# Kernel tuning notes

Measured on AMD Instinct MI355X. Metric: run time of the kernel, lower is better.

## Reference

```python
import math
import jax, jax.numpy as jnp
import numpy as np

B, N, DIM, H = 2, 4096, 1024, 16
DH = DIM // H
LEVELS = int(math.log2(N))
SCALE = 1.0 / math.sqrt(DH)


def build_lookup_table(seq_len):
    """Replicates build_hierarchical_index_lookup_table (numpy, static)."""
    levels = int(math.log2(seq_len))
    total_nodes = 2 * seq_len - 1
    max_valid = total_nodes - 2
    idx = np.full((seq_len, levels), -1, dtype=np.int32)
    cm = np.zeros((seq_len, levels), dtype=bool)
    for n in range(seq_len):
        nc = n
        for l in range(levels):
            if l == 0:
                pair = nc
                nn = nc ^ 1
            else:
                pair = nc // 2 + seq_len
                nn = pair ^ 1  # (nc//2 + seq_len) ^ 1 per Python precedence
            if nn > max_valid:
                break
            if pair < nn:
                cm[n, l] = True  # neighbor is to the right -> causally masked
            idx[n, l] = nn
            nc = nn
    return idx, cm


def setup_inputs() -> dict:
    key = jax.random.key(0)
    ks = jax.random.split(key, 12)
    w = lambda k: (jax.random.normal(k, (DIM, DIM), dtype=jnp.float32) * 0.02)
    idx_np, cm_np = build_lookup_table(N)
    return {
        "x": jax.random.normal(ks[0], (B, N, DIM), dtype=jnp.float32),
        "Wq_y": w(ks[1]), "Wk_y": w(ks[2]), "Wv_y": w(ks[3]),
        "Wo_y": w(ks[4]), "bo_y": jnp.zeros((DIM,), jnp.float32),
        "Wq_x": w(ks[5]), "Wk_x": w(ks[6]), "Wv_x": w(ks[7]),
        "Wo_x": w(ks[8]), "bo_x": jnp.zeros((DIM,), jnp.float32),
        "idx_map": jnp.asarray(idx_np, dtype=jnp.int32),       # [N, LEVELS]
        "causal_mask": jnp.asarray(cm_np, dtype=jnp.bool_),    # [N, LEVELS]
    }


def _heads(t):
    b, n, _ = t.shape
    return t.reshape(b, n, H, DH)


def _forward(x, Wq_y, Wk_y, Wv_y, Wo_y, bo_y, Wq_x, Wk_x, Wv_x, Wo_x, bo_x,
             idx_map, causal_mask):
    # ---- stage 1: build parent nodes level by level (online 2-child softmax merge)
    nodes = [x]  # leaves: [B, N, DIM]; parents appended level by level
    cur = x
    for _ in range(LEVELS):
        pre = 0.5 * (cur[:, 0::2] + cur[:, 1::2])     # parent query source [B,P,DIM]
        q = _heads(pre @ Wq_y)                        # [B,P,H,DH]
        k = _heads(cur @ Wk_y)                        # [B,C,H,DH]
        v = _heads(cur @ Wv_y)
        s0 = jnp.einsum('bphd,bphd->bph', q, k[:, 0::2]) * SCALE
        s1 = jnp.einsum('bphd,bphd->bph', q, k[:, 1::2]) * SCALE
        m = jnp.maximum(s0, s1)
        e0 = jnp.exp(s0 - m)
        e1 = jnp.exp(s1 - m)
        denom = e0 + e1 + 1e-9
        parent = ((e0 / denom)[..., None] * v[:, 0::2]
                  + (e1 / denom)[..., None] * v[:, 1::2])   # [B,P,H,DH]
        bp, pp = parent.shape[0], parent.shape[1]
        parent = parent.reshape(bp, pp, DIM) @ Wo_y + bo_y
        nodes.append(parent)
        cur = parent
    h_all = jnp.concatenate(nodes, axis=1)            # [B, 2N-1, DIM]

    # ---- stage 2: fused multi-level gather attention over self + neighbors
    Q = _heads(x @ Wq_x)                              # leaf queries [B,N,H,DH]
    K_all = _heads(h_all @ Wk_x)                      # [B,2N-1,H,DH]
    V_all = _heads(h_all @ Wv_x)

    k_cross = jnp.take(K_all, idx_map, axis=1)        # [B,N,LEVELS,H,DH]
    v_cross = jnp.take(V_all, idx_map, axis=1)

    s_self = jnp.einsum('bnhd,bnhd->bnh', Q, K_all[:, :N]) * SCALE   # [B,N,H]
    s_cross = jnp.einsum('bnhd,bnlhd->bnhl', Q, k_cross) * SCALE     # [B,N,H,L]
    neg_inf = jnp.float32(-jnp.inf)
    s_cross = jnp.where(causal_mask[None, :, None, :], neg_inf, s_cross)

    scores = jnp.concatenate([s_self[..., None], s_cross], axis=-1)  # [B,N,H,L+1]
    w = jax.nn.softmax(scores, axis=-1)
    out = (w[..., 0:1] * V_all[:, :N]
           + jnp.einsum('bnhl,bnlhd->bnhd', w[..., 1:], v_cross))    # [B,N,H,DH]
    return out.reshape(B, N, DIM) @ Wo_x + bo_x


def reference(x, Wq_y, Wk_y, Wv_y, Wo_y, bo_y, Wq_x, Wk_x, Wv_x, Wo_x, bo_x,
              idx_map, causal_mask):
    return _forward(x, Wq_y, Wk_y, Wv_y, Wo_y, bo_y,
                    Wq_x, Wk_x, Wv_x, Wo_x, bo_x, idx_map, causal_mask)
```

## Files before the change

### kernel.cpp

```cpp
#include <hip/hip_runtime.h>
#include <stdint.h>

#define H_NODES 8191
#define NN 4096
#define DIMC 1024

typedef __bf16 bf16x8 __attribute__((ext_vector_type(8)));
typedef float f32x4 __attribute__((ext_vector_type(4)));

__device__ __forceinline__ float b2f(ushort u) {
  union { uint32_t i; float f; } x; x.i = ((uint32_t)u) << 16; return x.f;
}
__device__ __forceinline__ ushort f2b(float f) {
  union { float f; uint32_t i; } x; x.f = f;
  uint32_t r = x.i + 0x7FFFu + ((x.i >> 16) & 1u);
  return (ushort)(r >> 16);
}
__device__ __forceinline__ void load16f(const ushort* p, float* f) {
  const uint32_t* w = (const uint32_t*)p;
  #pragma unroll
  for (int i = 0; i < 8; ++i) {
    uint32_t v = w[i];
    f[2 * i]     = b2f((ushort)(v & 0xffff));
    f[2 * i + 1] = b2f((ushort)(v >> 16));
  }
}
__device__ __forceinline__ void store16b(ushort* p, const float* f) {
  uint32_t w[8];
  #pragma unroll
  for (int i = 0; i < 8; ++i)
    w[i] = (uint32_t)f2b(f[2 * i]) | ((uint32_t)f2b(f[2 * i + 1]) << 16);
  *(uint4*)p = *(const uint4*)&w[0];
  *(uint4*)(p + 8) = *(const uint4*)&w[4];
}

struct WPtrs { const float* w[8]; };

__global__ void __launch_bounds__(256) transpose_w_k(WPtrs wp, ushort* __restrict__ dst) {
  __shared__ float t[32][33];
  const float* src = wp.w[blockIdx.z];
  int c0 = blockIdx.x * 32, r0 = blockIdx.y * 32;
  int tx = threadIdx.x, ty = threadIdx.y;
  #pragma unroll
  for (int i = ty; i < 32; i += 8)
    t[i][tx] = src[(long)(r0 + i) * DIMC + c0 + tx];
  __syncthreads();
  ushort* d = dst + (long)blockIdx.z * DIMC * DIMC;
  #pragma unroll
  for (int i = ty; i < 32; i += 8)
    d[(long)(c0 + i) * DIMC + r0 + tx] = f2b(t[tx][i]);
}

__global__ void __launch_bounds__(256) cvt_x_k(const float* __restrict__ x, ushort* __restrict__ h) {
  long t = (long)blockIdx.x * 256 + threadIdx.x;
  long i = t << 2;
  if (i >= (long)2 * NN * DIMC) return;
  long row = i >> 10;
  int col = (int)(i & 1023);
  long b = row >> 12;
  long n = row & 4095;
  float4 v = *(const float4*)(x + i);
  ushort* d = h + ((b * H_NODES + n) << 10) + col;
  uint2 pk;
  pk.x = (uint32_t)f2b(v.x) | ((uint32_t)f2b(v.y) << 16);
  pk.y = (uint32_t)f2b(v.z) | ((uint32_t)f2b(v.w) << 16);
  *(uint2*)d = pk;
}

__global__ void __launch_bounds__(256) avg_pairs_k(const ushort* __restrict__ h,
    ushort* __restrict__ pre, int P, int offL) {
  long t = (long)blockIdx.x * 256 + threadIdx.x;
  if (t >= (long)2 * P * 128) return;
  int dblk = (int)(t & 127);
  long r = t >> 7;
  int b = (r >= P) ? 1 : 0;
  int p = (int)(r - (long)b * P);
  const ushort* c = h + (((long)(b * H_NODES + offL + 2 * p)) << 10) + dblk * 8;
  const uint4 a0 = *(const uint4*)c;
  const uint4 a1 = *(const uint4*)(c + DIMC);
  const uint32_t* pa = (const uint32_t*)&a0;
  const uint32_t* pb = (const uint32_t*)&a1;
  uint32_t outw[4];
  #pragma unroll
  for (int i = 0; i < 4; ++i) {
    float x0 = b2f((ushort)(pa[i] & 0xffff)), x1 = b2f((ushort)(pa[i] >> 16));
    float y0 = b2f((ushort)(pb[i] & 0xffff)), y1 = b2f((ushort)(pb[i] >> 16));
    ushort r0 = f2b(0.5f * (x0 + y0)), r1 = f2b(0.5f * (x1 + y1));
    outw[i] = (uint32_t)r0 | ((uint32_t)r1 << 16);
  }
  *(uint4*)(pre + (((long)(b * P + p)) << 10) + dblk * 8) = *(const uint4*)outw;
}

struct GemmDesc {
  const ushort* A; long sAb;
  const ushort* Bt;
  const float* bias;
  void* C; long sCb; int ldc;
  int M; int outMode;
  int tX, tY;
  ushort* preC;
  long sPreB;
};

__device__ __forceinline__ void stage_tile(const GemmDesc& d, const ushort* Ab,
    int row0, int col0, ushort* lA, ushort* lB, int kt, int wave, int lane) {
  #pragma unroll
  for (int j = 0; j < 2; ++j) {
    int s = wave * 128 + j * 64 + lane;
    int r = s >> 2;
    int g = (s & 3) ^ ((r >> 1) & 3);
    int gr = row0 + r; gr = (gr < d.M) ? gr : (d.M - 1);
    const ushort* srcA = Ab + (long)gr * DIMC + kt * 32 + g * 8;
    __builtin_amdgcn_global_load_lds(
        (const __attribute__((address_space(1))) void*)(uintptr_t)srcA,
        (__attribute__((address_space(3))) void*)(uint32_t)(uintptr_t)(lA + (wave * 128 + j * 64) * 8),
        16, 0, 0);
    const ushort* srcB = d.Bt + (long)(col0 + r) * DIMC + kt * 32 + g * 8;
    __builtin_amdgcn_global_load_lds(
        (const __attribute__((address_space(1))) void*)(uintptr_t)srcB,
        (__attribute__((address_space(3))) void*)(uint32_t)(uintptr_t)(lB + (wave * 128 + j * 64) * 8),
        16, 0, 0);
  }
}

__device__ __forceinline__ void gemm_tile(const GemmDesc& d, int bz, int row0, int col0,
    ushort* lA, ushort* lB, int tid) {
  const ushort* Ab = d.A + (long)bz * d.sAb;
  int wave = tid >> 6, lane = tid & 63;
  int wr = wave >> 1, wc = wave & 1;

  f32x4 acc[4][4];
  #pragma unroll
  for (int m = 0; m < 4; ++m)
    #pragma unroll
    for (int n = 0; n < 4; ++n) acc[m][n] = (f32x4){0.f, 0.f, 0.f, 0.f};

  int rr = lane & 15, g4 = lane >> 4;
  for (int kt = 0; kt < 32; ++kt) {
    stage_tile(d, Ab, row0, col0, lA, lB, kt, wave, lane);
    __syncthreads();
    bf16x8 af[4], bfr[4];
    #pragma unroll
    for (int m = 0; m < 4; ++m) {
      int r = wr * 64 + m * 16 + rr;
      int slot = g4 ^ ((r >> 1) & 3);
      af[m] = *reinterpret_cast<const bf16x8*>(&lA[r * 32 + slot * 8]);
    }
    #pragma unroll
    for (int n = 0; n < 4; ++n) {
      int r = wc * 64 + n * 16 + rr;
      int slot = g4 ^ ((r >> 1) & 3);
      bfr[n] = *reinterpret_cast<const bf16x8*>(&lB[r * 32 + slot * 8]);
    }
    #pragma unroll
    for (int m = 0; m < 4; ++m)
      #pragma unroll
      for (int n = 0; n < 4; ++n)
        acc[m][n] = __builtin_amdgcn_mfma_f32_16x16x32_bf16(af[m], bfr[n], acc[m][n], 0, 0, 0);
    __syncthreads();
  }

  int rq = lane >> 4;
  #pragma unroll
  for (int n = 0; n < 4; ++n) {
    int col = col0 + wc * 64 + n * 16 + rr;
    float bv = d.bias ? d.bias[col] : 0.0f;
    #pragma unroll
    for (int m = 0; m < 4; ++m) {
      int gr0 = row0 + wr * 64 + m * 16 + rq * 4;
      float vv[4];
      #pragma unroll
      for (int r = 0; r < 4; ++r) vv[r] = acc[m][n][r] + bv;
      #pragma unroll
      for (int r = 0; r < 4; ++r) {
        int gr = gr0 + r;
        if (gr < d.M) {
          long o = (long)bz * d.sCb + (long)gr * d.ldc + col;
          if (d.outMode == 2) ((float*)d.C)[o] = vv[r];
          else ((ushort*)d.C)[o] = f2b(vv[r]);
        }
      }
      if (d.preC) {
        #pragma unroll
        for (int r = 0; r < 4; r += 2) {
          int gr = gr0 + r;
          if (gr + 1 < d.M)
            d.preC[(long)bz * d.sPreB + (long)(gr >> 1) * DIMC + col] =
                f2b(0.5f * (vv[r] + vv[r + 1]));
        }
      }
    }
  }
}

__global__ void __launch_bounds__(256, 4) gemm_multi(GemmDesc d0, GemmDesc d1, int t0) {
  __shared__ __align__(16) ushort lA[4096];
  __shared__ __align__(16) ushort lB[4096];
  int t = blockIdx.x;
  const GemmDesc& d = (t < t0) ? d0 : d1;
  int u = (t < t0) ? t : t - t0;
  int per = d.tX * d.tY;
  int bz = u / per;
  int rem = u - bz * per;
  int ty = rem / d.tX;
  int tx = rem - ty * d.tX;
  gemm_tile(d, bz, tx * 128, ty * 128, lA, lB, threadIdx.x);
}

__global__ void __launch_bounds__(256) merge_y2_k(const ushort* __restrict__ q,
    const ushort* __restrict__ kv, ushort* __restrict__ outp, int P) {
  int wave = threadIdx.x >> 6, lane = threadIdx.x & 63;
  long w = (long)blockIdx.x * 4 + wave;
  if (w >= (long)2 * P) return;
  int b = (w >= P) ? 1 : 0;
  int p = (int)(w - (long)b * P);
  const ushort* qp = q + (((long)(b * P + p)) << 10) + lane * 16;
  const ushort* kvb = kv + ((long)(b * 2 * P + 2 * p)) * 2048;
  float qf[16], k0f[16], k1f[16];
  load16f(qp, qf);
  load16f(kvb + lane * 16, k0f);
  load16f(kvb + 2048 + lane * 16, k1f);
  float d0 = 0.f, d1 = 0.f;
  #pragma unroll
  for (int j = 0; j < 16; ++j) { d0 += qf[j] * k0f[j]; d1 += qf[j] * k1f[j]; }
  d0 += __shfl_xor(d0, 1); d0 += __shfl_xor(d0, 2);
  d1 += __shfl_xor(d1, 1); d1 += __shfl_xor(d1, 2);
  float s0 = d0 * 0.125f, s1 = d1 * 0.125f;
  float mm = fmaxf(s0, s1);
  float e0 = expf(s0 - mm), e1 = expf(s1 - mm);
  float inv = 1.0f / (e0 + e1 + 1e-9f);
  float w0 = e0 * inv, w1 = e1 * inv;
  float v0f[16], v1f[16], ov[16];
  load16f(kvb + 1024 + lane * 16, v0f);
  load16f(kvb + 2048 + 1024 + lane * 16, v1f);
  #pragma unroll
  for (int j = 0; j < 16; ++j) ov[j] = w0 * v0f[j] + w1 * v1f[j];
  store16b(outp + (((long)(b * P + p)) << 10) + lane * 16, ov);
}

__global__ void __launch_bounds__(256) attn_x2_k(const ushort* __restrict__ Q,
    const ushort* __restrict__ KV, ushort* __restrict__ outp) {
  int wave = threadIdx.x >> 6, lane = threadIdx.x & 63;
  long w = (long)blockIdx.x * 4 + wave;
  int n = (int)(w & 4095);
  int b = (int)(w >> 12);
  const ushort* KVb = KV + (long)b * H_NODES * 2048;
  float qf[16];
  load16f(Q + (((long)b * NN + n) << 10) + lane * 16, qf);
  int nb[13];
  nb[0] = n;
  #pragma unroll
  for (int l = 0; l < 12; ++l) nb[1 + l] = (8192 - (8192 >> l)) + ((n >> l) ^ 1);
  float s[13];
  #pragma unroll
  for (int i = 0; i < 13; ++i) {
    float kf[16];
    load16f(KVb + (long)nb[i] * 2048 + lane * 16, kf);
    float d = 0.f;
    #pragma unroll
    for (int j = 0; j < 16; ++j) d += qf[j] * kf[j];
    d += __shfl_xor(d, 1);
    d += __shfl_xor(d, 2);
    s[i] = d * 0.125f;
  }
  #pragma unroll
  for (int l = 0; l < 12; ++l)
    if (((n >> l) & 1) == 0) s[1 + l] = -__builtin_inff();
  float mm = s[0];
  #pragma unroll
  for (int i = 1; i < 13; ++i) mm = fmaxf(mm, s[i]);
  float e[13], sum = 0.f;
  #pragma unroll
  for (int i = 0; i < 13; ++i) { e[i] = expf(s[i] - mm); sum += e[i]; }
  float inv = 1.0f / sum;
  float ov[16];
  #pragma unroll
  for (int j = 0; j < 16; ++j) ov[j] = 0.f;
  #pragma unroll
  for (int i = 0; i < 13; ++i) {
    float wgt = e[i] * inv;
    float vf[16];
    load16f(KVb + (long)nb[i] * 2048 + 1024 + lane * 16, vf);
    #pragma unroll
    for (int j = 0; j < 16; ++j) ov[j] += wgt * vf[j];
  }
  store16b(outp + (((long)b * NN + n) << 10) + lane * 16, ov);
}

extern "C" void kernel_launch(void* const* d_in, const int* in_sizes, int n_in,
                              void* d_out, int out_size, void* d_ws, size_t ws_size,
                              hipStream_t stream) {
  const float* x    = (const float*)d_in[0];
  const float* Wq_y = (const float*)d_in[1];
  const float* Wk_y = (const float*)d_in[2];
  const float* Wv_y = (const float*)d_in[3];
  const float* Wo_y = (const float*)d_in[4];
  const float* bo_y = (const float*)d_in[5];
  const float* Wq_x = (const float*)d_in[6];
  const float* Wk_x = (const float*)d_in[7];
  const float* Wv_x = (const float*)d_in[8];
  const float* Wo_x = (const float*)d_in[9];
  const float* bo_x = (const float*)d_in[10];

  ushort* wt  = (ushort*)d_ws;
  ushort* h   = wt + (size_t)8 * 1024 * 1024;
  ushort* reg = h + (size_t)2 * H_NODES * DIMC;
  ushort* Qx   = reg;
  ushort* KVa  = Qx + (size_t)2 * 4096 * DIMC;
  ushort* aout = KVa + (size_t)2 * H_NODES * 2048;
  ushort* preB = aout;
  ushort* qbB  = preB + (size_t)2 * 2048 * DIMC;
  ushort* kv1B = qbB + (size_t)2 * 2048 * DIMC;
  ushort* mrgB = kv1B + (size_t)2 * 4096 * 2048;
  ushort* preS = preB;
  ushort* qbS  = qbB;
  ushort* kv1S = kv1B;
  ushort* mrgS = mrgB;

  size_t wsElems = (size_t)8 * 1024 * 1024 + (size_t)2 * H_NODES * DIMC +
                   (size_t)2 * 4096 * DIMC + (size_t)2 * H_NODES * 2048 +
                   ((size_t)2 * 2048 * DIMC * 2 + (size_t)2 * 4096 * 2048 +
                    (size_t)2 * 2048 * DIMC);
  if (ws_size < wsElems * 2) return;

  WPtrs wp;
  wp.w[0] = Wq_y; wp.w[1] = Wk_y; wp.w[2] = Wv_y; wp.w[3] = Wo_y;
  wp.w[4] = Wq_x; wp.w[5] = Wk_x; wp.w[6] = Wv_x; wp.w[7] = Wo_x;
  transpose_w_k<<<dim3(32, 32, 8), dim3(32, 8), 0, stream>>>(wp, wt);
  cvt_x_k<<<8192, 256, 0, stream>>>(x, h);
  avg_pairs_k<<<(2 * 2048 * 128 + 255) / 256, 256, 0, stream>>>(h, preB, 2048, 0);

  auto mk128 = [](const ushort* A, long sAb, const ushort* Bt, const float* bias,
                  void* C, long sCb, int ldc, int M, int outMode, int tY) {
    GemmDesc d; d.A = A; d.sAb = sAb; d.Bt = Bt; d.bias = bias; d.C = C; d.sCb = sCb;
    d.ldc = ldc; d.M = M; d.outMode = outMode; d.tX = (M + 127) / 128; d.tY = tY;
    d.preC = nullptr; d.sPreB = 0;
    return d;
  };
  auto kvSub = [&](long start, int len) {
    return mk128(h + start * DIMC, (long)H_NODES * DIMC, wt + (size_t)5 * 1024 * 1024,
                 nullptr, KVa + start * 2048, (long)H_NODES * 2048, 2048, len, 0, 16);
  };
  auto qSub = [&](long start, int len) {
    return mk128(h + start * DIMC, (long)H_NODES * DIMC, wt + (size_t)4 * 1024 * 1024,
                 nullptr, Qx + start * DIMC, (long)4096 * DIMC, DIMC, len, 0, 8);
  };

  for (int l = 0; l < 12; ++l) {
    int P = NN >> (l + 1);
    int offL = 8192 - (8192 >> l);
    int offP = 8192 - (8192 >> (l + 1));
    ushort* pre = (l >= 3) ? preS : preB;
    ushort* qb  = (l >= 3) ? qbS  : qbB;
    ushort* kv1 = (l >= 3) ? kv1S : kv1B;
    ushort* mrg = (l >= 3) ? mrgS : mrgB;

    GemmDesc dq  = mk128(pre, (long)P * DIMC, wt, nullptr,
                         qb, (long)P * DIMC, DIMC, P, 0, 8);
    GemmDesc dkv = mk128(h + (long)offL * DIMC, (long)H_NODES * DIMC,
                         wt + (size_t)1 * 1024 * 1024, nullptr,
                         kv1, (long)2 * P * 2048, 2048, 2 * P, 0, 16);
    int t0 = dq.tX * dq.tY * 2;
    gemm_multi<<<t0 + dkv.tX * dkv.tY * 2, 256, 0, stream>>>(dq, dkv, t0);

    merge_y2_k<<<(2 * P + 3) / 4, 256, 0, stream>>>(qb, kv1, mrg, P);

    GemmDesc dgo = mk128(mrg, (long)P * DIMC, wt + (size_t)3 * 1024 * 1024, bo_y,
                         h + (long)offP * DIMC, (long)H_NODES * DIMC, DIMC, P, 1, 8);
    if (l < 11) {
      dgo.preC = (l >= 2) ? preS : preB;
      dgo.sPreB = (long)(P / 2) * DIMC;
    }
    GemmDesc att = dgo; int nAtt = 0;
    if      (l == 0)  att = qSub(0, 2048);
    else if (l == 1)  att = qSub(2048, 2048);
    else if (l == 2)  att = kvSub(0, 1792);
    else if (l == 3)  att = kvSub(1792, 1920);
    else if (l == 4)  att = kvSub(3712, 1920);
    else if (l == 5)  att = kvSub(5632, 1536);
    else if (l == 6)  att = kvSub(7168, 512);
    else if (l == 7)  att = kvSub(7680, 256);
    else if (l == 8)  att = kvSub(7936, 128);
    else if (l == 9)  att = kvSub(8064, 64);
    else if (l == 10) att = kvSub(8128, 32);
    else if (l == 11) att = kvSub(8160, 16);
    nAtt = att.tX * att.tY * 2;
    int n0 = dgo.tX * dgo.tY * 2;
    gemm_multi<<<n0 + nAtt, 256, 0, stream>>>(dgo, att, n0);
  }

  {
    GemmDesc a0 = kvSub(8176, 8), a1 = kvSub(8184, 7);
    int n0 = a0.tX * a0.tY * 2, n1 = a1.tX * a1.tY * 2;
    gemm_multi<<<n0 + n1, 256, 0, stream>>>(a0, a1, n0);
  }
  attn_x2_k<<<2048, 256, 0, stream>>>(Qx, KVa, aout);
  {
    GemmDesc dox = mk128(aout, (long)4096 * DIMC, wt + (size_t)7 * 1024 * 1024, bo_x,
                         d_out, (long)4096 * DIMC, DIMC, 4096, 2, 8);
    gemm_multi<<<dox.tX * dox.tY * 2, 256, 0, stream>>>(dox, dox, dox.tX * dox.tY * 2);
  }
}
```

Measured before the change: 753.9 us.

## Double-buffer GEMM LDS tiles with BK=64 and async prefetch

The GEMM main loop moves from a single-buffered 32-wide K tile with two syncthreads per step to a double-buffered 64-wide K tile. The next tile is prefetched via global_load_lds while the current one feeds the MFMAs, with vmcnt waits and raw barriers replacing the full syncs. The LDS swizzle is changed to an 8-slot XOR pattern and s_setprio raises priority around the MFMA bursts. LDS use grows from 16KB to 64KB per block and the occupancy hint in launch_bounds is dropped, so fewer blocks can be resident per CU.

```diff
diff --git a/kernel.cpp b/kernel.cpp
--- a/kernel.cpp
+++ b/kernel.cpp
@@ -105,26 +105,26 @@
 __device__ __forceinline__ void stage_tile(const GemmDesc& d, const ushort* Ab,
     int row0, int col0, ushort* lA, ushort* lB, int kt, int wave, int lane) {
   #pragma unroll
-  for (int j = 0; j < 2; ++j) {
-    int s = wave * 128 + j * 64 + lane;
-    int r = s >> 2;
-    int g = (s & 3) ^ ((r >> 1) & 3);
+  for (int j = 0; j < 4; ++j) {
+    int s = wave * 256 + j * 64 + lane;
+    int r = s >> 3, slot = s & 7;
+    int gb = slot ^ (r & 7);
     int gr = row0 + r; gr = (gr < d.M) ? gr : (d.M - 1);
-    const ushort* srcA = Ab + (long)gr * DIMC + kt * 32 + g * 8;
+    const ushort* srcA = Ab + (long)gr * DIMC + kt * 64 + gb * 8;
     __builtin_amdgcn_global_load_lds(
         (const __attribute__((address_space(1))) void*)(uintptr_t)srcA,
-        (__attribute__((address_space(3))) void*)(uint32_t)(uintptr_t)(lA + (wave * 128 + j * 64) * 8),
+        (__attribute__((address_space(3))) void*)(uint32_t)(uintptr_t)(lA + s * 8),
         16, 0, 0);
-    const ushort* srcB = d.Bt + (long)(col0 + r) * DIMC + kt * 32 + g * 8;
+    const ushort* srcB = d.Bt + (long)(col0 + r) * DIMC + kt * 64 + gb * 8;
     __builtin_amdgcn_global_load_lds(
         (const __attribute__((address_space(1))) void*)(uintptr_t)srcB,
-        (__attribute__((address_space(3))) void*)(uint32_t)(uintptr_t)(lB + (wave * 128 + j * 64) * 8),
+        (__attribute__((address_space(3))) void*)(uint32_t)(uintptr_t)(lB + s * 8),
         16, 0, 0);
   }
 }
 
 __device__ __forceinline__ void gemm_tile(const GemmDesc& d, int bz, int row0, int col0,
-    ushort* lA, ushort* lB, int tid) {
+    ushort (*lA)[8192], ushort (*lB)[8192], int tid) {
   const ushort* Ab = d.A + (long)bz * d.sAb;
   int wave = tid >> 6, lane = tid & 63;
   int wr = wave >> 1, wc = wave & 1;
@@ -135,29 +135,42 @@
     #pragma unroll
     for (int n = 0; n < 4; ++n) acc[m][n] = (f32x4){0.f, 0.f, 0.f, 0.f};
 
+  stage_tile(d, Ab, row0, col0, lA[0], lB[0], 0, wave, lane);
+
   int rr = lane & 15, g4 = lane >> 4;
-  for (int kt = 0; kt < 32; ++kt) {
-    stage_tile(d, Ab, row0, col0, lA, lB, kt, wave, lane);
-    __syncthreads();
-    bf16x8 af[4], bfr[4];
+  for (int kt = 0; kt < 16; ++kt) {
+    int cur = kt & 1;
+    if (kt + 1 < 16) {
+      stage_tile(d, Ab, row0, col0, lA[cur ^ 1], lB[cur ^ 1], kt + 1, wave, lane);
+      asm volatile("s_waitcnt vmcnt(8)" ::: "memory");
+    } else {
+      asm volatile("s_waitcnt vmcnt(0)" ::: "memory");
+    }
+    __builtin_amdgcn_s_barrier();
     #pragma unroll
-    for (int m = 0; m < 4; ++m) {
-      int r = wr * 64 + m * 16 + rr;
-      int slot = g4 ^ ((r >> 1) & 3);
-      af[m] = *reinterpret_cast<const bf16x8*>(&lA[r * 32 + slot * 8]);
+    for (int ks = 0; ks < 2; ++ks) {
+      bf16x8 af[4], bfr[4];
+      #pragma unroll
+      for (int m = 0; m < 4; ++m) {
+        int r = wr * 64 + m * 16 + rr;
+        int slot = (ks * 4 + g4) ^ (r & 7);
+        af[m] = *reinterpret_cast<const bf16x8*>(&lA[cur][r * 64 + slot * 8]);
+      }
+      #pragma unroll
+      for (int n = 0; n < 4; ++n) {
+        int r = wc * 64 + n * 16 + rr;
+        int slot = (ks * 4 + g4) ^ (r & 7);
+        bfr[n] = *reinterpret_cast<const bf16x8*>(&lB[cur][r * 64 + slot * 8]);
+      }
+      __builtin_amdgcn_s_setprio(1);
+      #pragma unroll
+      for (int m = 0; m < 4; ++m)
+        #pragma unroll
+        for (int n = 0; n < 4; ++n)
+          acc[m][n] = __builtin_amdgcn_mfma_f32_16x16x32_bf16(af[m], bfr[n], acc[m][n], 0, 0, 0);
+      __builtin_amdgcn_s_setprio(0);
     }
-    #pragma unroll
-    for (int n = 0; n < 4; ++n) {
-      int r = wc * 64 + n * 16 + rr;
-      int slot = g4 ^ ((r >> 1) & 3);
-      bfr[n] = *reinterpret_cast<const bf16x8*>(&lB[r * 32 + slot * 8]);
-    }
-    #pragma unroll
-    for (int m = 0; m < 4; ++m)
-      #pragma unroll
-      for (int n = 0; n < 4; ++n)
-        acc[m][n] = __builtin_amdgcn_mfma_f32_16x16x32_bf16(af[m], bfr[n], acc[m][n], 0, 0, 0);
-    __syncthreads();
+    __builtin_amdgcn_s_barrier();
   }
 
   int rq = lane >> 4;
@@ -193,9 +206,9 @@
   }
 }
 
-__global__ void __launch_bounds__(256, 4) gemm_multi(GemmDesc d0, GemmDesc d1, int t0) {
-  __shared__ __align__(16) ushort lA[4096];
-  __shared__ __align__(16) ushort lB[4096];
+__global__ void __launch_bounds__(256) gemm_multi(GemmDesc d0, GemmDesc d1, int t0) {
+  __shared__ __align__(16) ushort lA[2][8192];
+  __shared__ __align__(16) ushort lB[2][8192];
   int t = blockIdx.x;
   const GemmDesc& d = (t < t0) ? d0 : d1;
   int u = (t < t0) ? t : t - t0;
```

Result: faster. 697.5 us (-7.5%).
